# Optimization experiments

Measured on AMD Instinct MI355X. Metric: run time of the kernel, lower is better.

## Reference

```python
import jax, jax.numpy as jnp
import numpy as np

C = 512  # in_channels

def setup_inputs() -> dict:
    key = jax.random.key(0)
    k1, k2 = jax.random.split(key)
    x = jax.random.normal(k1, (16, C, 16384), dtype=jnp.float32)
    weight = jax.random.normal(k2, (C, C), dtype=jnp.float32)
    return {"x": x, "weight": weight}

def _cayley(A):
    # Q = (I + A)^{-1} (I - A), A skew-symmetric -> Q orthogonal
    I = jnp.eye(A.shape[-1], dtype=A.dtype)
    return jnp.linalg.solve(I + A, I - A)

def reference(x, weight):
    A = weight - weight.T              # skew-symmetric parametrization
    K = _cayley(A)                     # [C, C] orthogonal kernel
    # 1x1 channel mixing: y[b,j,n] = sum_i K[j,i] x[b,i,n]
    y = jnp.einsum('ji,bin->bjn', K, x)
    return y
```

## Files before the change

kernel.cpp:

```cpp
#include <hip/hip_runtime.h>
#include <hip/hip_cooperative_groups.h>

namespace cg = cooperative_groups;

typedef __attribute__((ext_vector_type(8))) short short8;
typedef __attribute__((ext_vector_type(4))) float f32x4;

#define CDIM 512
#define NSEQ 16384

__device__ __forceinline__ unsigned short f2bf(float f) {
    unsigned u = __float_as_uint(f);
    unsigned r = ((u >> 16) & 1u) + 0x7fffu;
    return (unsigned short)((u + r) >> 16);
}

__device__ __forceinline__ void gll16(const void* g, void* l) {
    __builtin_amdgcn_global_load_lds((const __attribute__((address_space(1))) unsigned int*)g,
                                     (__attribute__((address_space(3))) unsigned int*)l,
                                     16, 0, 0);
}

__global__ __launch_bounds__(512, 1) void cayley_kernel(const float* __restrict__ W,
                                                        float* __restrict__ G,
                                                        float* __restrict__ Dinv,
                                                        float* __restrict__ Pbuf,
                                                        unsigned short* __restrict__ Kb) {
    cg::grid_group gg = cg::this_grid();
    __shared__ union {
        struct { float prow[2][256]; float pcol[2][128]; } inv;
        struct { float ins[128][64]; float dch[128][33]; } rs;
        struct { float Lt[64][129]; float Pt[128][64]; } tr;
    } sm;

    int t = threadIdx.x;
    int bid = blockIdx.x;
    int gtid = bid * 512 + t;

    for (int e = gtid; e < 512 * 1024; e += 128 * 512) {
        int r = e >> 10, c = e & 1023;
        float v;
        if (c < 512) {
            float a = W[r * 512 + c] - W[c * 512 + r];
            v = (c == r ? 1.f : 0.f) + a;
        } else {
            int c2 = c - 512;
            float a = W[r * 512 + c2] - W[c2 * 512 + r];
            v = (c2 == r ? 1.f : 0.f) - a;
        }
        G[e] = v;
    }
    gg.sync();

    for (int k = 0; k < 4; k++) {
        int ck = k * 128;
        int nct = (896 - 128 * k) >> 6;

        if (bid == 0) {
            int c0 = t & 63, rg = t >> 6;
            float rgs[16][4];
#pragma unroll
            for (int m = 0; m < 16; m++) {
                int r = rg + 8 * m;
#pragma unroll
                for (int q = 0; q < 4; q++) {
                    int c = c0 + 64 * q;
                    rgs[m][q] = (c < 128) ? G[(size_t)(ck + r) * 1024 + ck + c]
                                          : ((r == c - 128) ? 1.f : 0.f);
                }
            }
            if (rg == 0) {
#pragma unroll
                for (int q = 0; q < 4; q++) sm.inv.prow[0][c0 + 64 * q] = rgs[0][q];
            }
            if (c0 == 0) {
#pragma unroll
                for (int m = 0; m < 16; m++) sm.inv.pcol[0][rg + 8 * m] = rgs[m][0];
            }
            __syncthreads();
            for (int p = 0; p < 128; p++) {
                int buf = p & 1;
                float inv = 1.0f / sm.inv.prow[buf][p];
                float pr[4];
#pragma unroll
                for (int q = 0; q < 4; q++) pr[q] = sm.inv.prow[buf][c0 + 64 * q];
#pragma unroll
                for (int m = 0; m < 16; m++) {
                    int r = rg + 8 * m;
                    if (r == p) {
#pragma unroll
                        for (int q = 0; q < 4; q++) rgs[m][q] = pr[q] * inv;
                    } else {
                        float f = sm.inv.pcol[buf][r] * inv;
#pragma unroll
                        for (int q = 0; q < 4; q++) rgs[m][q] -= f * pr[q];
                    }
                }
                if (p < 127) {
                    int p2 = p + 1, nb = p2 & 1;
                    int mp = p2 >> 3, qp = p2 >> 6;
                    if (rg == (p2 & 7)) {
#pragma unroll
                        for (int m = 0; m < 16; m++)
                            if (m == mp) {
#pragma unroll
                                for (int q = 0; q < 4; q++)
                                    sm.inv.prow[nb][c0 + 64 * q] = rgs[m][q];
                            }
                    }
                    if (c0 == (p2 & 63)) {
#pragma unroll
                        for (int q = 0; q < 4; q++)
                            if (q == qp) {
#pragma unroll
                                for (int m = 0; m < 16; m++)
                                    sm.inv.pcol[nb][rg + 8 * m] = rgs[m][q];
                            }
                    }
                }
                __syncthreads();
            }
#pragma unroll
            for (int m = 0; m < 16; m++) {
                Dinv[(rg + 8 * m) * 128 + c0] = rgs[m][2];
                Dinv[(rg + 8 * m) * 128 + c0 + 64] = rgs[m][3];
            }
        }
        gg.sync();

        if (bid < nct) {
            int cbase = ck + 128 + bid * 64;
            for (int idx = t; idx < 128 * 64; idx += 512) {
                int r = idx >> 6, c = idx & 63;
                sm.rs.ins[r][c] = G[(size_t)(ck + r) * 1024 + cbase + c];
            }
            int tx = t & 15, ty = t >> 4;
            float acc[4][4];
#pragma unroll
            for (int i = 0; i < 4; i++)
#pragma unroll
                for (int j = 0; j < 4; j++) acc[i][j] = 0.f;
            for (int mc = 0; mc < 4; mc++) {
                __syncthreads();
                for (int idx = t; idx < 128 * 32; idx += 512) {
                    int r = idx >> 5, c = idx & 31;
                    sm.rs.dch[r][c] = Dinv[r * 128 + mc * 32 + c];
                }
                __syncthreads();
                for (int m2 = 0; m2 < 32; m2++) {
                    int mm = mc * 32 + m2;
                    float p0 = sm.rs.ins[mm][tx * 4 + 0], p1 = sm.rs.ins[mm][tx * 4 + 1];
                    float p2 = sm.rs.ins[mm][tx * 4 + 2], p3 = sm.rs.ins[mm][tx * 4 + 3];
#pragma unroll
                    for (int rr = 0; rr < 4; rr++) {
                        float d = sm.rs.dch[ty * 4 + rr][m2];
                        acc[rr][0] += d * p0;
                        acc[rr][1] += d * p1;
                        acc[rr][2] += d * p2;
                        acc[rr][3] += d * p3;
                    }
                }
            }
#pragma unroll
            for (int rr = 0; rr < 4; rr++)
#pragma unroll
                for (int cc = 0; cc < 4; cc++)
                    Pbuf[(ty * 4 + rr) * 896 + bid * 64 + tx * 4 + cc] = acc[rr][cc];
        }
        gg.sync();

        {
            int ct = bid >> 3, rt = bid & 7;
            if (ct < nct) {
                int cbase = ck + 128 + ct * 64;
                int rb = rt * 64;
                bool pivot = (rb >= ck) && (rb < ck + 128);
                if (pivot) {
                    for (int idx = t; idx < 64 * 64; idx += 512) {
                        int r = idx >> 6, c = idx & 63;
                        G[(size_t)(rb + r) * 1024 + cbase + c] =
                            Pbuf[(rb - ck + r) * 896 + ct * 64 + c];
                    }
                } else {
                    for (int idx = t; idx < 64 * 128; idx += 512) {
                        int r = idx >> 7, c = idx & 127;
                        sm.tr.Lt[r][c] = G[(size_t)(rb + r) * 1024 + ck + c];
                    }
                    for (int idx = t; idx < 128 * 64; idx += 512) {
                        int r = idx >> 6, c = idx & 63;
                        sm.tr.Pt[r][c] = Pbuf[r * 896 + ct * 64 + c];
                    }
                    __syncthreads();
                    int tx = t & 15, ty = t >> 4;
                    float acc[2][4];
#pragma unroll
                    for (int i = 0; i < 2; i++)
#pragma unroll
                        for (int j = 0; j < 4; j++) acc[i][j] = 0.f;
                    for (int mm = 0; mm < 128; mm++) {
                        float p0 = sm.tr.Pt[mm][tx * 4 + 0], p1 = sm.tr.Pt[mm][tx * 4 + 1];
                        float p2 = sm.tr.Pt[mm][tx * 4 + 2], p3 = sm.tr.Pt[mm][tx * 4 + 3];
                        float l0 = sm.tr.Lt[ty * 2 + 0][mm], l1 = sm.tr.Lt[ty * 2 + 1][mm];
                        acc[0][0] += l0 * p0; acc[0][1] += l0 * p1;
                        acc[0][2] += l0 * p2; acc[0][3] += l0 * p3;
                        acc[1][0] += l1 * p0; acc[1][1] += l1 * p1;
                        acc[1][2] += l1 * p2; acc[1][3] += l1 * p3;
                    }
#pragma unroll
                    for (int rr = 0; rr < 2; rr++)
#pragma unroll
                        for (int cc = 0; cc < 4; cc++)
                            G[(size_t)(rb + ty * 2 + rr) * 1024 + cbase + tx * 4 + cc] -=
                                acc[rr][cc];
                }
            }
        }
        gg.sync();
    }

    {
        int e = gtid * 4;
        int j = e >> 9, i = e & 511;
        const float* src = G + (size_t)j * 1024 + 512 + i;
        unsigned short* dst = Kb + j * 512 + i;
        float v0 = src[0], v1 = src[1], v2 = src[2], v3 = src[3];
        uint2 pk;
        pk.x = f2bf(v0) | ((unsigned)f2bf(v1) << 16);
        pk.y = f2bf(v2) | ((unsigned)f2bf(v3) << 16);
        *(uint2*)dst = pk;
    }
}

__global__ void buildG_kernel(const float* __restrict__ W, float* __restrict__ G) {
    int r = blockIdx.x;
    for (int c = threadIdx.x; c < 1024; c += 256) {
        float v;
        if (c < 512) {
            float a = W[r * 512 + c] - W[c * 512 + r];
            v = (c == r ? 1.f : 0.f) + a;
        } else {
            int c2 = c - 512;
            float a = W[r * 512 + c2] - W[c2 * 512 + r];
            v = (c2 == r ? 1.f : 0.f) - a;
        }
        G[(size_t)r * 1024 + c] = v;
    }
}

__global__ __launch_bounds__(512) void invdiag_kernel(float* __restrict__ G,
                                                      float* __restrict__ Dinv, int k) {
    int ck = k * 128;
    __shared__ float prow[2][256];
    __shared__ float pcol[2][128];
    int t = threadIdx.x;
    int c0 = t & 63, rg = t >> 6;
    float rgs[16][4];
#pragma unroll
    for (int m = 0; m < 16; m++) {
        int r = rg + 8 * m;
#pragma unroll
        for (int q = 0; q < 4; q++) {
            int c = c0 + 64 * q;
            rgs[m][q] = (c < 128) ? G[(size_t)(ck + r) * 1024 + ck + c]
                                  : ((r == c - 128) ? 1.f : 0.f);
        }
    }
    if (rg == 0) {
#pragma unroll
        for (int q = 0; q < 4; q++) prow[0][c0 + 64 * q] = rgs[0][q];
    }
    if (c0 == 0) {
#pragma unroll
        for (int m = 0; m < 16; m++) pcol[0][rg + 8 * m] = rgs[m][0];
    }
    __syncthreads();
    for (int p = 0; p < 128; p++) {
        int buf = p & 1;
        float inv = 1.0f / prow[buf][p];
        float pr[4];
#pragma unroll
        for (int q = 0; q < 4; q++) pr[q] = prow[buf][c0 + 64 * q];
#pragma unroll
        for (int m = 0; m < 16; m++) {
            int r = rg + 8 * m;
            if (r == p) {
#pragma unroll
                for (int q = 0; q < 4; q++) rgs[m][q] = pr[q] * inv;
            } else {
                float f = pcol[buf][r] * inv;
#pragma unroll
                for (int q = 0; q < 4; q++) rgs[m][q] -= f * pr[q];
            }
        }
        if (p < 127) {
            int p2 = p + 1, nb = p2 & 1;
            int mp = p2 >> 3, qp = p2 >> 6;
            if (rg == (p2 & 7)) {
#pragma unroll
                for (int m = 0; m < 16; m++)
                    if (m == mp) {
#pragma unroll
                        for (int q = 0; q < 4; q++) prow[nb][c0 + 64 * q] = rgs[m][q];
                    }
            }
            if (c0 == (p2 & 63)) {
#pragma unroll
                for (int q = 0; q < 4; q++)
                    if (q == qp) {
#pragma unroll
                        for (int m = 0; m < 16; m++) pcol[nb][rg + 8 * m] = rgs[m][q];
                    }
            }
        }
        __syncthreads();
    }
#pragma unroll
    for (int m = 0; m < 16; m++) {
        Dinv[(rg + 8 * m) * 128 + c0] = rgs[m][2];
        Dinv[(rg + 8 * m) * 128 + c0 + 64] = rgs[m][3];
    }
}

__global__ void rowscale_kernel(float* __restrict__ G, const float* __restrict__ Dinv,
                                int k) {
    int ck = k * 128;
    int cbase = ck + 128 + blockIdx.x * 64;
    __shared__ float ins[128][64];
    __shared__ float dch[128][33];
    int t = threadIdx.x;
    for (int idx = t; idx < 128 * 64; idx += 256) {
        int r = idx >> 6, c = idx & 63;
        ins[r][c] = G[(size_t)(ck + r) * 1024 + cbase + c];
    }
    int tx = t & 15, ty = t >> 4;
    float acc[8][4];
#pragma unroll
    for (int i = 0; i < 8; i++)
#pragma unroll
        for (int j = 0; j < 4; j++) acc[i][j] = 0.f;
    for (int mc = 0; mc < 4; mc++) {
        __syncthreads();
        for (int idx = t; idx < 128 * 32; idx += 256) {
            int r = idx >> 5, c = idx & 31;
            dch[r][c] = Dinv[r * 128 + mc * 32 + c];
        }
        __syncthreads();
        for (int m2 = 0; m2 < 32; m2++) {
            int mm = mc * 32 + m2;
            float p0 = ins[mm][tx * 4 + 0], p1 = ins[mm][tx * 4 + 1];
            float p2 = ins[mm][tx * 4 + 2], p3 = ins[mm][tx * 4 + 3];
#pragma unroll
            for (int rr = 0; rr < 8; rr++) {
                float d = dch[ty * 8 + rr][m2];
                acc[rr][0] += d * p0;
                acc[rr][1] += d * p1;
                acc[rr][2] += d * p2;
                acc[rr][3] += d * p3;
            }
        }
    }
#pragma unroll
    for (int rr = 0; rr < 8; rr++)
#pragma unroll
        for (int cc = 0; cc < 4; cc++)
            G[(size_t)(ck + ty * 8 + rr) * 1024 + cbase + tx * 4 + cc] = acc[rr][cc];
}

__global__ void trailing_kernel(float* __restrict__ G, int k) {
    int ck = k * 128;
    int rb = blockIdx.x * 32;
    if (rb >= ck) rb += 128;
    int cbase = ck + 128 + blockIdx.y * 64;
    __shared__ float Lt[32][129];
    __shared__ float Pt[128][64];
    int t = threadIdx.x;
    for (int idx = t; idx < 32 * 128; idx += 256) {
        int r = idx >> 7, c = idx & 127;
        Lt[r][c] = G[(size_t)(rb + r) * 1024 + ck + c];
    }
    for (int idx = t; idx < 128 * 64; idx += 256) {
        int r = idx >> 6, c = idx & 63;
        Pt[r][c] = G[(size_t)(ck + r) * 1024 + cbase + c];
    }
    __syncthreads();
    int tx = t & 15, ty = t >> 4;
    float acc[2][4];
#pragma unroll
    for (int i = 0; i < 2; i++)
#pragma unroll
        for (int j = 0; j < 4; j++) acc[i][j] = 0.f;
    for (int mm = 0; mm < 128; mm++) {
        float p0 = Pt[mm][tx * 4 + 0], p1 = Pt[mm][tx * 4 + 1];
        float p2 = Pt[mm][tx * 4 + 2], p3 = Pt[mm][tx * 4 + 3];
        float l0 = Lt[ty * 2 + 0][mm], l1 = Lt[ty * 2 + 1][mm];
        acc[0][0] += l0 * p0; acc[0][1] += l0 * p1; acc[0][2] += l0 * p2; acc[0][3] += l0 * p3;
        acc[1][0] += l1 * p0; acc[1][1] += l1 * p1; acc[1][2] += l1 * p2; acc[1][3] += l1 * p3;
    }
#pragma unroll
    for (int rr = 0; rr < 2; rr++)
#pragma unroll
        for (int cc = 0; cc < 4; cc++)
            G[(size_t)(rb + ty * 2 + rr) * 1024 + cbase + tx * 4 + cc] -= acc[rr][cc];
}

__global__ void cvtK_kernel(const float* __restrict__ G, unsigned short* __restrict__ Kb) {
    int idx = blockIdx.x * 256 + threadIdx.x;
    int e = idx * 4;
    int j = e >> 9, i = e & 511;
    const float* src = G + (size_t)j * 1024 + 512 + i;
    unsigned short* dst = Kb + j * 512 + i;
    float v0 = src[0], v1 = src[1], v2 = src[2], v3 = src[3];
    uint2 pk;
    pk.x = f2bf(v0) | ((unsigned)f2bf(v1) << 16);
    pk.y = f2bf(v2) | ((unsigned)f2bf(v3) << 16);
    *(uint2*)dst = pk;
}

#define LDX 40

__global__ __launch_bounds__(512, 2) void gemm_kernel(const float* __restrict__ x,
                                                      const unsigned short* __restrict__ Kb,
                                                      float* __restrict__ y) {
    __shared__ unsigned short kt[2][512 * 32];
    __shared__ unsigned short xt[2][64 * LDX];
    int t = threadIdx.x;
    int l = t & 63, w = t >> 6;
    int bx = blockIdx.x;
    int b = bx >> 8;
    int n0 = (bx & 255) << 6;
    const float* xb = x + (size_t)b * CDIM * NSEQ + n0;
    float* yb = y + (size_t)b * CDIM * NSEQ + n0;

    int lr = l & 15;
    int q8 = (l >> 4) * 8;
    int kidx = q8 ^ ((lr & 3) << 3);

    const char* kgl = (const char*)Kb + (size_t)(64 * w + (l >> 2)) * 1024 +
                      (((l & 3) * 16) ^ (((l >> 2) & 3) << 4));

    f32x4 acc[4][4];
#pragma unroll
    for (int i = 0; i < 4; i++)
#pragma unroll
        for (int j = 0; j < 4; j++) acc[i][j] = (f32x4){0.f, 0.f, 0.f, 0.f};

    {
        unsigned short* kdst = kt[0] + w * 64 * 32;
#pragma unroll
        for (int i = 0; i < 4; i++) gll16(kgl + i * 16384, kdst + i * 16 * 32);
        const float* xs = xb + (size_t)(w * 4) * NSEQ + l;
        uint2 pk;
        pk.x = f2bf(__builtin_nontemporal_load(xs)) |
               ((unsigned)f2bf(__builtin_nontemporal_load(xs + NSEQ)) << 16);
        pk.y = f2bf(__builtin_nontemporal_load(xs + 2 * NSEQ)) |
               ((unsigned)f2bf(__builtin_nontemporal_load(xs + 3 * NSEQ)) << 16);
        *(uint2*)(xt[0] + l * LDX + w * 4) = pk;
    }

    for (int s = 0; s < 16; s++) {
        const unsigned short* ktc = kt[s & 1];
        const unsigned short* xtc = xt[s & 1];
        __syncthreads();

        float v0, v1, v2, v3;
        if (s < 15) {
            unsigned short* kdst = kt[(s + 1) & 1] + w * 64 * 32;
#pragma unroll
            for (int i = 0; i < 4; i++)
                gll16(kgl + (size_t)(s + 1) * 64 + i * 16384, kdst + i * 16 * 32);
            const float* xs = xb + (size_t)((s + 1) * 32 + w * 4) * NSEQ + l;
            v0 = __builtin_nontemporal_load(xs);
            v1 = __builtin_nontemporal_load(xs + NSEQ);
            v2 = __builtin_nontemporal_load(xs + 2 * NSEQ);
            v3 = __builtin_nontemporal_load(xs + 3 * NSEQ);
        }

        short8 af[4], bfr[4];
#pragma unroll
        for (int mt = 0; mt < 4; mt++)
            af[mt] = *(const short8*)(ktc + (w * 64 + mt * 16 + lr) * 32 + kidx);
#pragma unroll
        for (int nt = 0; nt < 4; nt++)
            bfr[nt] = *(const short8*)(xtc + (nt * 16 + lr) * LDX + q8);
#pragma unroll
        for (int mt = 0; mt < 4; mt++)
#pragma unroll
            for (int nt = 0; nt < 4; nt++)
                acc[mt][nt] = __builtin_amdgcn_mfma_f32_16x16x32_bf16(af[mt], bfr[nt],
                                                                      acc[mt][nt], 0, 0, 0);

        if (s < 15) {
            uint2 pk;
            pk.x = f2bf(v0) | ((unsigned)f2bf(v1) << 16);
            pk.y = f2bf(v2) | ((unsigned)f2bf(v3) << 16);
            *(uint2*)(xt[(s + 1) & 1] + l * LDX + w * 4) = pk;
        }
    }

    int qr = (l >> 4) * 4;
#pragma unroll
    for (int mt = 0; mt < 4; mt++)
#pragma unroll
        for (int nt = 0; nt < 4; nt++)
#pragma unroll
            for (int r = 0; r < 4; r++)
                __builtin_nontemporal_store(
                    acc[mt][nt][r],
                    &yb[(size_t)(w * 64 + mt * 16 + qr + r) * NSEQ + nt * 16 + lr]);
}

extern "C" void kernel_launch(void* const* d_in, const int* in_sizes, int n_in,
                              void* d_out, int out_size, void* d_ws, size_t ws_size,
                              hipStream_t stream) {
    const float* x = (const float*)d_in[0];
    const float* W = (const float*)d_in[1];
    float* y = (float*)d_out;

    float* G = (float*)d_ws;
    float* DINV = (float*)((char*)d_ws + 0x200000);
    float* PB = (float*)((char*)d_ws + 0x210000);
    unsigned short* KB = (unsigned short*)((char*)d_ws + 0x280000);

    const float* Wp = W;
    float* Gp = G;
    float* Dp = DINV;
    float* Pp = PB;
    unsigned short* Kp = KB;
    void* args[] = {(void*)&Wp, (void*)&Gp, (void*)&Dp, (void*)&Pp, (void*)&Kp};
    hipError_t ce = hipLaunchCooperativeKernel((void*)cayley_kernel, dim3(128), dim3(512),
                                               args, 0, stream);
    if (ce != hipSuccess) {
        buildG_kernel<<<512, 256, 0, stream>>>(W, G);
        for (int k = 0; k < 4; k++) {
            invdiag_kernel<<<1, 512, 0, stream>>>(G, DINV, k);
            int ncols = 896 - 128 * k;
            rowscale_kernel<<<ncols / 64, 256, 0, stream>>>(G, DINV, k);
            trailing_kernel<<<dim3(12, ncols / 64), 256, 0, stream>>>(G, k);
        }
        cvtK_kernel<<<256, 256, 0, stream>>>(G, KB);
    }
    gemm_kernel<<<4096, 512, 0, stream>>>(x, KB, y);
}
```

Baseline: 1.998 ms.

## Overlap x bf16 transpose-conversion with Cayley solve in one cooperative kernel

The cooperative pre-kernel is split by block index. 64 blocks run the Cayley LU solve using a custom atomic grid barrier. The other 192 blocks convert x to bf16 in a transposed [n][c] layout in workspace at the same time. The GEMM then loads bf16 x tiles straight into LDS with global_load_lds, so the per-step fp32 loads and conversion in registers go away. The cost is an extra 256MB write and read pass through HBM for xT, plus fewer blocks doing the solve. The fallback path keeps the old fp32-x GEMM.

```diff
diff --git a/kernel.cpp b/kernel.cpp
--- a/kernel.cpp
+++ b/kernel.cpp
@@ -1,7 +1,4 @@
 #include <hip/hip_runtime.h>
-#include <hip/hip_cooperative_groups.h>
-
-namespace cg = cooperative_groups;
 
 typedef __attribute__((ext_vector_type(8))) short short8;
 typedef __attribute__((ext_vector_type(4))) float f32x4;
@@ -21,23 +18,70 @@
                                      16, 0, 0);
 }
 
-__global__ __launch_bounds__(512, 1) void cayley_kernel(const float* __restrict__ W,
-                                                        float* __restrict__ G,
-                                                        float* __restrict__ Dinv,
-                                                        float* __restrict__ Pbuf,
-                                                        unsigned short* __restrict__ Kb) {
-    cg::grid_group gg = cg::this_grid();
+__device__ __forceinline__ void gbarrier(unsigned* cnt, unsigned* gen, unsigned nblk) {
+    __syncthreads();
+    if (threadIdx.x == 0) {
+        unsigned g = __hip_atomic_load(gen, __ATOMIC_RELAXED, __HIP_MEMORY_SCOPE_AGENT);
+        unsigned a =
+            __hip_atomic_fetch_add(cnt, 1u, __ATOMIC_ACQ_REL, __HIP_MEMORY_SCOPE_AGENT);
+        if (a == nblk - 1u) {
+            __hip_atomic_store(cnt, 0u, __ATOMIC_RELAXED, __HIP_MEMORY_SCOPE_AGENT);
+            __hip_atomic_fetch_add(gen, 1u, __ATOMIC_RELEASE, __HIP_MEMORY_SCOPE_AGENT);
+        } else {
+            while (__hip_atomic_load(gen, __ATOMIC_ACQUIRE, __HIP_MEMORY_SCOPE_AGENT) == g)
+                __builtin_amdgcn_s_sleep(2);
+        }
+    }
+    __syncthreads();
+}
+
+__global__ __launch_bounds__(512, 1) void fused_pre_kernel(
+    const float* __restrict__ x, const float* __restrict__ W, float* __restrict__ G,
+    float* __restrict__ Dinv, float* __restrict__ Pbuf, unsigned short* __restrict__ Kb,
+    unsigned short* __restrict__ xT, unsigned* __restrict__ bar) {
     __shared__ union {
         struct { float prow[2][256]; float pcol[2][128]; } inv;
         struct { float ins[128][64]; float dch[128][33]; } rs;
         struct { float Lt[64][129]; float Pt[128][64]; } tr;
+        struct { float tile[64][129]; } cv;
     } sm;
 
     int t = threadIdx.x;
     int bid = blockIdx.x;
-    int gtid = bid * 512 + t;
-
-    for (int e = gtid; e < 512 * 1024; e += 128 * 512) {
+
+    if (bid >= 64) {
+        for (int tile = bid - 64; tile < 16384; tile += 192) {
+            int b = tile >> 10, rem = tile & 1023;
+            int i0 = (rem >> 7) << 6, n0 = (rem & 127) << 7;
+            __syncthreads();
+            for (int k2 = t; k2 < 64 * 128; k2 += 512) {
+                int i = k2 >> 7, n = k2 & 127;
+                sm.cv.tile[i][n] = x[((size_t)b * 512 + i0 + i) * NSEQ + n0 + n];
+            }
+            __syncthreads();
+#pragma unroll
+            for (int r = 0; r < 2; r++) {
+                int task = t + (r << 9);
+                int n = task >> 3, oc = task & 7;
+                float v0 = sm.cv.tile[oc * 8 + 0][n], v1 = sm.cv.tile[oc * 8 + 1][n];
+                float v2 = sm.cv.tile[oc * 8 + 2][n], v3 = sm.cv.tile[oc * 8 + 3][n];
+                float v4 = sm.cv.tile[oc * 8 + 4][n], v5 = sm.cv.tile[oc * 8 + 5][n];
+                float v6 = sm.cv.tile[oc * 8 + 6][n], v7 = sm.cv.tile[oc * 8 + 7][n];
+                uint4 pk;
+                pk.x = f2bf(v0) | ((unsigned)f2bf(v1) << 16);
+                pk.y = f2bf(v2) | ((unsigned)f2bf(v3) << 16);
+                pk.z = f2bf(v4) | ((unsigned)f2bf(v5) << 16);
+                pk.w = f2bf(v6) | ((unsigned)f2bf(v7) << 16);
+                *(uint4*)(xT + ((size_t)b * NSEQ + n0 + n) * 512 + i0 + oc * 8) = pk;
+            }
+        }
+        return;
+    }
+
+    unsigned* cnt = bar;
+    unsigned* gen = bar + 1;
+
+    for (int e = bid * 512 + t; e < 512 * 1024; e += 64 * 512) {
         int r = e >> 10, c = e & 1023;
         float v;
         if (c < 512) {
@@ -50,7 +94,7 @@
         }
         G[e] = v;
     }
-    gg.sync();
+    gbarrier(cnt, gen, 64);
 
     for (int k = 0; k < 4; k++) {
         int ck = k * 128;
@@ -126,7 +170,7 @@
                 Dinv[(rg + 8 * m) * 128 + c0 + 64] = rgs[m][3];
             }
         }
-        gg.sync();
+        gbarrier(cnt, gen, 64);
 
         if (bid < nct) {
             int cbase = ck + 128 + bid * 64;
@@ -167,68 +211,143 @@
                 for (int cc = 0; cc < 4; cc++)
                     Pbuf[(ty * 4 + rr) * 896 + bid * 64 + tx * 4 + cc] = acc[rr][cc];
         }
-        gg.sync();
-
-        {
-            int ct = bid >> 3, rt = bid & 7;
-            if (ct < nct) {
-                int cbase = ck + 128 + ct * 64;
-                int rb = rt * 64;
-                bool pivot = (rb >= ck) && (rb < ck + 128);
-                if (pivot) {
-                    for (int idx = t; idx < 64 * 64; idx += 512) {
-                        int r = idx >> 6, c = idx & 63;
-                        G[(size_t)(rb + r) * 1024 + cbase + c] =
-                            Pbuf[(rb - ck + r) * 896 + ct * 64 + c];
-                    }
-                } else {
-                    for (int idx = t; idx < 64 * 128; idx += 512) {
-                        int r = idx >> 7, c = idx & 127;
-                        sm.tr.Lt[r][c] = G[(size_t)(rb + r) * 1024 + ck + c];
-                    }
-                    for (int idx = t; idx < 128 * 64; idx += 512) {
-                        int r = idx >> 6, c = idx & 63;
-                        sm.tr.Pt[r][c] = Pbuf[r * 896 + ct * 64 + c];
-                    }
-                    __syncthreads();
-                    int tx = t & 15, ty = t >> 4;
-                    float acc[2][4];
-#pragma unroll
-                    for (int i = 0; i < 2; i++)
-#pragma unroll
-                        for (int j = 0; j < 4; j++) acc[i][j] = 0.f;
-                    for (int mm = 0; mm < 128; mm++) {
-                        float p0 = sm.tr.Pt[mm][tx * 4 + 0], p1 = sm.tr.Pt[mm][tx * 4 + 1];
-                        float p2 = sm.tr.Pt[mm][tx * 4 + 2], p3 = sm.tr.Pt[mm][tx * 4 + 3];
-                        float l0 = sm.tr.Lt[ty * 2 + 0][mm], l1 = sm.tr.Lt[ty * 2 + 1][mm];
-                        acc[0][0] += l0 * p0; acc[0][1] += l0 * p1;
-                        acc[0][2] += l0 * p2; acc[0][3] += l0 * p3;
-                        acc[1][0] += l1 * p0; acc[1][1] += l1 * p1;
-                        acc[1][2] += l1 * p2; acc[1][3] += l1 * p3;
-                    }
-#pragma unroll
-                    for (int rr = 0; rr < 2; rr++)
-#pragma unroll
-                        for (int cc = 0; cc < 4; cc++)
-                            G[(size_t)(rb + ty * 2 + rr) * 1024 + cbase + tx * 4 + cc] -=
-                                acc[rr][cc];
-                }
-            }
-        }
-        gg.sync();
-    }
-
-    {
-        int e = gtid * 4;
+        gbarrier(cnt, gen, 64);
+
+        for (int tl = bid; tl < nct * 8; tl += 64) {
+            int ct = tl >> 3, rt = tl & 7;
+            int cbase = ck + 128 + ct * 64;
+            int rb = rt * 64;
+            bool pivot = (rb >= ck) && (rb < ck + 128);
+            __syncthreads();
+            if (pivot) {
+                for (int idx = t; idx < 64 * 64; idx += 512) {
+                    int r = idx >> 6, c = idx & 63;
+                    G[(size_t)(rb + r) * 1024 + cbase + c] =
+                        Pbuf[(rb - ck + r) * 896 + ct * 64 + c];
+                }
+            } else {
+                for (int idx = t; idx < 64 * 128; idx += 512) {
+                    int r = idx >> 7, c = idx & 127;
+                    sm.tr.Lt[r][c] = G[(size_t)(rb + r) * 1024 + ck + c];
+                }
+                for (int idx = t; idx < 128 * 64; idx += 512) {
+                    int r = idx >> 6, c = idx & 63;
+                    sm.tr.Pt[r][c] = Pbuf[r * 896 + ct * 64 + c];
+                }
+                __syncthreads();
+                int tx = t & 15, ty = t >> 4;
+                float acc[2][4];
+#pragma unroll
+                for (int i = 0; i < 2; i++)
+#pragma unroll
+                    for (int j = 0; j < 4; j++) acc[i][j] = 0.f;
+                for (int mm = 0; mm < 128; mm++) {
+                    float p0 = sm.tr.Pt[mm][tx * 4 + 0], p1 = sm.tr.Pt[mm][tx * 4 + 1];
+                    float p2 = sm.tr.Pt[mm][tx * 4 + 2], p3 = sm.tr.Pt[mm][tx * 4 + 3];
+                    float l0 = sm.tr.Lt[ty * 2 + 0][mm], l1 = sm.tr.Lt[ty * 2 + 1][mm];
+                    acc[0][0] += l0 * p0; acc[0][1] += l0 * p1;
+                    acc[0][2] += l0 * p2; acc[0][3] += l0 * p3;
+                    acc[1][0] += l1 * p0; acc[1][1] += l1 * p1;
+                    acc[1][2] += l1 * p2; acc[1][3] += l1 * p3;
+                }
+#pragma unroll
+                for (int rr = 0; rr < 2; rr++)
+#pragma unroll
+                    for (int cc = 0; cc < 4; cc++)
+                        G[(size_t)(rb + ty * 2 + rr) * 1024 + cbase + tx * 4 + cc] -=
+                            acc[rr][cc];
+            }
+        }
+        gbarrier(cnt, gen, 64);
+    }
+
+    for (int g2 = bid * 512 + t; g2 < 65536; g2 += 64 * 512) {
+        int e = g2 * 4;
         int j = e >> 9, i = e & 511;
         const float* src = G + (size_t)j * 1024 + 512 + i;
-        unsigned short* dst = Kb + j * 512 + i;
         float v0 = src[0], v1 = src[1], v2 = src[2], v3 = src[3];
         uint2 pk;
         pk.x = f2bf(v0) | ((unsigned)f2bf(v1) << 16);
         pk.y = f2bf(v2) | ((unsigned)f2bf(v3) << 16);
-        *(uint2*)dst = pk;
-    }
+        *(uint2*)(Kb + j * 512 + i) = pk;
+    }
+}
+
+__global__ __launch_bounds__(512, 2) void gemm_bf16_kernel(
+    const unsigned short* __restrict__ xT, const unsigned short* __restrict__ Kb,
+    float* __restrict__ y) {
+    __shared__ unsigned short kt[2][512 * 32];
+    __shared__ unsigned short xt[2][64 * 32];
+    int t = threadIdx.x;
+    int l = t & 63, w = t >> 6;
+    int bx = blockIdx.x;
+    int b = bx >> 8;
+    int n0 = (bx & 255) << 6;
+    float* yb = y + (size_t)b * CDIM * NSEQ + n0;
+
+    int lr = l & 15;
+    int g = l >> 4;
+    int q8 = g * 8;
+    int kidx = q8 ^ ((lr & 3) << 3);
+    int xidx = q8 ^ (((lr >> 1) & 3) << 3);
+
+    const char* kgl = (const char*)Kb + (size_t)(64 * w + (l >> 2)) * 1024 +
+                      (((l & 3) * 16) ^ (((l >> 2) & 3) << 4));
+    const char* xgl =
+        (const char*)xT + ((size_t)((size_t)b * NSEQ + n0 + 16 * w + (l >> 2)) * 512 +
+                           (((l & 3) ^ ((l >> 3) & 3)) * 8)) *
+                              2;
+
+    f32x4 acc[4][4];
+#pragma unroll
+    for (int i = 0; i < 4; i++)
+#pragma unroll
+        for (int j = 0; j < 4; j++) acc[i][j] = (f32x4){0.f, 0.f, 0.f, 0.f};
+
+    {
+        unsigned short* kdst = kt[0] + w * 2048;
+#pragma unroll
+        for (int i = 0; i < 4; i++) gll16(kgl + i * 16384, kdst + i * 512);
+        if (w < 4) gll16(xgl, xt[0] + w * 512);
+    }
+
+    for (int s = 0; s < 16; s++) {
+        const unsigned short* ktc = kt[s & 1];
+        const unsigned short* xtc = xt[s & 1];
+        __syncthreads();
+
+        if (s < 15) {
+            unsigned short* kdst = kt[(s + 1) & 1] + w * 2048;
+#pragma unroll
+            for (int i = 0; i < 4; i++)
+                gll16(kgl + (s + 1) * 64 + i * 16384, kdst + i * 512);
+            if (w < 4) gll16(xgl + (s + 1) * 64, xt[(s + 1) & 1] + w * 512);
+        }
+
+        short8 af[4], bfr[4];
+#pragma unroll
+        for (int mt = 0; mt < 4; mt++)
+            af[mt] = *(const short8*)(ktc + (w * 64 + mt * 16 + lr) * 32 + kidx);
+#pragma unroll
+        for (int nt = 0; nt < 4; nt++)
+            bfr[nt] = *(const short8*)(xtc + (nt * 16 + lr) * 32 + xidx);
+#pragma unroll
+        for (int mt = 0; mt < 4; mt++)
+#pragma unroll
+            for (int nt = 0; nt < 4; nt++)
+                acc[mt][nt] = __builtin_amdgcn_mfma_f32_16x16x32_bf16(af[mt], bfr[nt],
+                                                                      acc[mt][nt], 0, 0, 0);
+    }
+
+    int qr = g * 4;
+#pragma unroll
+    for (int mt = 0; mt < 4; mt++)
+#pragma unroll
+        for (int nt = 0; nt < 4; nt++)
+#pragma unroll
+            for (int r = 0; r < 4; r++)
+                yb[(size_t)(w * 64 + mt * 16 + qr + r) * NSEQ + nt * 16 + lr] =
+                    acc[mt][nt][r];
 }
 
 __global__ void buildG_kernel(const float* __restrict__ W, float* __restrict__ G) {
@@ -408,19 +527,17 @@
     int e = idx * 4;
     int j = e >> 9, i = e & 511;
     const float* src = G + (size_t)j * 1024 + 512 + i;
-    unsigned short* dst = Kb + j * 512 + i;
     float v0 = src[0], v1 = src[1], v2 = src[2], v3 = src[3];
     uint2 pk;
     pk.x = f2bf(v0) | ((unsigned)f2bf(v1) << 16);
     pk.y = f2bf(v2) | ((unsigned)f2bf(v3) << 16);
-    *(uint2*)dst = pk;
+    *(uint2*)(Kb + j * 512 + i) = pk;
 }
 
 #define LDX 40
-
-__global__ __launch_bounds__(512, 2) void gemm_kernel(const float* __restrict__ x,
-                                                      const unsigned short* __restrict__ Kb,
-                                                      float* __restrict__ y) {
+__global__ __launch_bounds__(512, 2) void gemm_f32x_kernel(
+    const float* __restrict__ x, const unsigned short* __restrict__ Kb,
+    float* __restrict__ y) {
     __shared__ unsigned short kt[2][512 * 32];
     __shared__ unsigned short xt[2][64 * LDX];
     int t = threadIdx.x;
@@ -430,51 +547,39 @@
     int n0 = (bx & 255) << 6;
     const float* xb = x + (size_t)b * CDIM * NSEQ + n0;
     float* yb = y + (size_t)b * CDIM * NSEQ + n0;
-
     int lr = l & 15;
     int q8 = (l >> 4) * 8;
     int kidx = q8 ^ ((lr & 3) << 3);
-
     const char* kgl = (const char*)Kb + (size_t)(64 * w + (l >> 2)) * 1024 +
                       (((l & 3) * 16) ^ (((l >> 2) & 3) << 4));
-
     f32x4 acc[4][4];
 #pragma unroll
     for (int i = 0; i < 4; i++)
 #pragma unroll
         for (int j = 0; j < 4; j++) acc[i][j] = (f32x4){0.f, 0.f, 0.f, 0.f};
-
     {
-        unsigned short* kdst = kt[0] + w * 64 * 32;
-#pragma unroll
-        for (int i = 0; i < 4; i++) gll16(kgl + i * 16384, kdst + i * 16 * 32);
+        unsigned short* kdst = kt[0] + w * 2048;
+#pragma unroll
+        for (int i = 0; i < 4; i++) gll16(kgl + i * 16384, kdst + i * 512);
         const float* xs = xb + (size_t)(w * 4) * NSEQ + l;
         uint2 pk;
-        pk.x = f2bf(__builtin_nontemporal_load(xs)) |
-               ((unsigned)f2bf(__builtin_nontemporal_load(xs + NSEQ)) << 16);
-        pk.y = f2bf(__builtin_nontemporal_load(xs + 2 * NSEQ)) |
-               ((unsigned)f2bf(__builtin_nontemporal_load(xs + 3 * NSEQ)) << 16);
+        pk.x = f2bf(xs[0]) | ((unsigned)f2bf(xs[NSEQ]) << 16);
+        pk.y = f2bf(xs[2 * NSEQ]) | ((unsigned)f2bf(xs[3 * NSEQ]) << 16);
         *(uint2*)(xt[0] + l * LDX + w * 4) = pk;
     }
-
     for (int s = 0; s < 16; s++) {
         const unsigned short* ktc = kt[s & 1];
         const unsigned short* xtc = xt[s & 1];
         __syncthreads();
-
         float v0, v1, v2, v3;
         if (s < 15) {
-            unsigned short* kdst = kt[(s + 1) & 1] + w * 64 * 32;
+            unsigned short* kdst = kt[(s + 1) & 1] + w * 2048;
 #pragma unroll
             for (int i = 0; i < 4; i++)
-                gll16(kgl + (size_t)(s + 1) * 64 + i * 16384, kdst + i * 16 * 32);
+                gll16(kgl + (s + 1) * 64 + i * 16384, kdst + i * 512);
             const float* xs = xb + (size_t)((s + 1) * 32 + w * 4) * NSEQ + l;
-            v0 = __builtin_nontemporal_load(xs);
-            v1 = __builtin_nontemporal_load(xs + NSEQ);
-            v2 = __builtin_nontemporal_load(xs + 2 * NSEQ);
-            v3 = __builtin_nontemporal_load(xs + 3 * NSEQ);
-        }
-
+            v0 = xs[0]; v1 = xs[NSEQ]; v2 = xs[2 * NSEQ]; v3 = xs[3 * NSEQ];
+        }
         short8 af[4], bfr[4];
 #pragma unroll
         for (int mt = 0; mt < 4; mt++)
@@ -488,7 +593,6 @@
             for (int nt = 0; nt < 4; nt++)
                 acc[mt][nt] = __builtin_amdgcn_mfma_f32_16x16x32_bf16(af[mt], bfr[nt],
                                                                       acc[mt][nt], 0, 0, 0);
-
         if (s < 15) {
             uint2 pk;
             pk.x = f2bf(v0) | ((unsigned)f2bf(v1) << 16);
@@ -496,7 +600,6 @@
             *(uint2*)(xt[(s + 1) & 1] + l * LDX + w * 4) = pk;
         }
     }
-
     int qr = (l >> 4) * 4;
 #pragma unroll
     for (int mt = 0; mt < 4; mt++)
@@ -504,9 +607,8 @@
         for (int nt = 0; nt < 4; nt++)
 #pragma unroll
             for (int r = 0; r < 4; r++)
-                __builtin_nontemporal_store(
-                    acc[mt][nt][r],
-                    &yb[(size_t)(w * 64 + mt * 16 + qr + r) * NSEQ + nt * 16 + lr]);
+                yb[(size_t)(w * 64 + mt * 16 + qr + r) * NSEQ + nt * 16 + lr] =
+                    acc[mt][nt][r];
 }
 
 extern "C" void kernel_launch(void* const* d_in, const int* in_sizes, int n_in,
@@ -520,16 +622,30 @@
     float* DINV = (float*)((char*)d_ws + 0x200000);
     float* PB = (float*)((char*)d_ws + 0x210000);
     unsigned short* KB = (unsigned short*)((char*)d_ws + 0x280000);
-
-    const float* Wp = W;
-    float* Gp = G;
-    float* Dp = DINV;
-    float* Pp = PB;
-    unsigned short* Kp = KB;
-    void* args[] = {(void*)&Wp, (void*)&Gp, (void*)&Dp, (void*)&Pp, (void*)&Kp};
-    hipError_t ce = hipLaunchCooperativeKernel((void*)cayley_kernel, dim3(128), dim3(512),
-                                               args, 0, stream);
-    if (ce != hipSuccess) {
+    unsigned* BAR = (unsigned*)((char*)d_ws + 0x300000);
+    unsigned short* XT = (unsigned short*)((char*)d_ws + 0x400000);
+
+    const size_t need = 0x400000 + (size_t)16 * NSEQ * CDIM * 2;
+    bool fused = ws_size >= need;
+
+    if (fused) {
+        hipMemsetAsync((char*)d_ws + 0x300000, 0, 64, stream);
+        const float* xp = x;
+        const float* Wp = W;
+        float* Gp = G;
+        float* Dp = DINV;
+        float* Pp = PB;
+        unsigned short* Kp = KB;
+        unsigned short* Xp = XT;
+        unsigned* Bp = BAR;
+        void* args[] = {(void*)&xp, (void*)&Wp, (void*)&Gp, (void*)&Dp,
+                        (void*)&Pp, (void*)&Kp, (void*)&Xp, (void*)&Bp};
+        hipError_t ce = hipLaunchCooperativeKernel((void*)fused_pre_kernel, dim3(256),
+                                                   dim3(512), args, 0, stream);
+        if (ce != hipSuccess) fused = false;
+    }
+
+    if (!fused) {
         buildG_kernel<<<512, 256, 0, stream>>>(W, G);
         for (int k = 0; k < 4; k++) {
             invdiag_kernel<<<1, 512, 0, stream>>>(G, DINV, k);
@@ -538,6 +654,8 @@
             trailing_kernel<<<dim3(12, ncols / 64), 256, 0, stream>>>(G, k);
         }
         cvtK_kernel<<<256, 256, 0, stream>>>(G, KB);
-    }
-    gemm_kernel<<<4096, 512, 0, stream>>>(x, KB, y);
-}
+        gemm_f32x_kernel<<<4096, 512, 0, stream>>>(x, KB, y);
+    } else {
+        gemm_bf16_kernel<<<4096, 512, 0, stream>>>(XT, KB, y);
+    }
+}
```

Result: faster. 1.957 ms (-2.0%).
